# Performance work log

Measured on AMD Instinct MI355X. Metric: run time of the kernel, lower is better.

## Reference

```python
import jax, jax.numpy as jnp
import numpy as np

NUM_HEADS = 16
INACTIVE = 4          # cfg_comp.attention_heads_inactive
SIG_DIM = 64          # cfg_comp.attention_heads_signature_dim
MLP_HIDDEN = 512      # cfg_comp.attention_heads_inference_mlp_hidden


def setup_inputs() -> dict:
    key = jax.random.key(0)
    ks = jax.random.split(key, 16)
    S, B, E = 2048, 2, 1024
    def xavier(k, shape, gain=1.0):
        fan_in, fan_out = shape[1], shape[0]
        a = gain * np.sqrt(6.0 / (fan_in + fan_out))
        return jax.random.uniform(k, shape, jnp.float32, -a, a)
    g = 1.0 / np.sqrt(2.0)
    return {
        "query": jax.random.normal(ks[0], (S, B, E), jnp.float32),
        "q_w": xavier(ks[1], (E, E), g), "q_b": jnp.zeros((E,), jnp.float32),
        "k_w": xavier(ks[2], (E, E), g), "k_b": jnp.zeros((E,), jnp.float32),
        "v_w": xavier(ks[3], (E, E), g), "v_b": jnp.zeros((E,), jnp.float32),
        "out_w": xavier(ks[4], (E, E)), "out_b": jnp.zeros((E,), jnp.float32),
        "inf1_w": xavier(ks[5], (MLP_HIDDEN, E), np.sqrt(2.0)),
        "inf1_b": jnp.zeros((MLP_HIDDEN,), jnp.float32),
        "inf2_w": xavier(ks[6], (SIG_DIM, MLP_HIDDEN), np.sqrt(2.0)),
        "inf2_b": jnp.zeros((SIG_DIM,), jnp.float32),
        "head_sig": jax.random.normal(ks[7], (NUM_HEADS, SIG_DIM), jnp.float32)
                    * np.sqrt(2.0 / (NUM_HEADS + SIG_DIM)),
    }


def _head_mask(query, inf1_w, inf1_b, inf2_w, inf2_b, head_sig):
    # inference_masking_step: (S, B, E) -> binary mask (B, H, S)
    t = jax.nn.relu(query @ inf1_w.T + inf1_b)          # (S, B, hidden)
    t = t @ inf2_w.T + inf2_b                            # (S, B, sig)
    s = t @ head_sig.T                                   # (S, B, H) head scores
    keep = NUM_HEADS - INACTIVE
    kth = jax.lax.top_k(s, keep)[0][..., -1]             # (S, B) kth-largest score
    mask = (s >= kth[..., None]).astype(query.dtype)     # 1 at top-`keep` heads
    mask = jax.lax.stop_gradient(mask)                   # scatter of constants in torch
    return jnp.transpose(mask, (1, 2, 0))                # (B, H, S)


def reference(query, q_w, q_b, k_w, k_b, v_w, v_b, out_w, out_b,
              inf1_w, inf1_b, inf2_w, inf2_b, head_sig):
    S, B, E = query.shape
    H, D = NUM_HEADS, E // NUM_HEADS
    scaling = D ** (-0.5)

    q = (query @ q_w.T + q_b) * scaling                  # (S, B, E)
    k = query @ k_w.T + k_b
    v = query @ v_w.T + v_b
    # (S, B, E) -> (B, H, S, D)
    to_bhsd = lambda x: jnp.transpose(x.reshape(S, B, H, D), (1, 2, 0, 3))
    q, k, v = to_bhsd(q), to_bhsd(k), to_bhsd(v)

    attn = jax.nn.softmax(jnp.einsum("bhqd,bhkd->bhqk", q, k), axis=-1)
    o = jnp.einsum("bhqk,bhkd->bhqd", attn, v)           # (B, H, S, D)

    mask = _head_mask(query, inf1_w, inf1_b, inf2_w, inf2_b, head_sig)  # (B, H, S)
    o = o * mask[..., None]                              # gate per head per position

    out = jnp.transpose(o, (2, 0, 1, 3)).reshape(S, B, E)
    return out @ out_w.T + out_b
```

## Files before the change

kernel.cpp:

```cpp
#include <hip/hip_runtime.h>
#include <hip/hip_bf16.h>

#define S_LEN 2048
#define BATCH 2
#define EDIM 1024
#define NHEAD 16
#define DHEAD 64
#define HIDDEN 512
#define SIGD 64
#define KEEP 12

typedef __attribute__((ext_vector_type(8))) short bf16x8;
typedef __attribute__((ext_vector_type(4))) float f32x4;

static __device__ __forceinline__ float bf2f(short s) {
  unsigned int u = ((unsigned int)(unsigned short)s) << 16;
  float f; __builtin_memcpy(&f, &u, 4); return f;
}
static __device__ __forceinline__ short f2bf(float f) {
  unsigned int u; __builtin_memcpy(&u, &f, 4);
  u += 0x7fffu + ((u >> 16) & 1u);
  return (short)(u >> 16);
}

#if __has_builtin(__builtin_amdgcn_exp2f)
static __device__ __forceinline__ float fexp2(float x) { return __builtin_amdgcn_exp2f(x); }
#else
static __device__ __forceinline__ float fexp2(float x) { return exp2f(x); }
#endif

static __device__ __forceinline__ void gl_lds16(const short* g, short* l) {
  __builtin_amdgcn_global_load_lds(
      (const __attribute__((address_space(1))) unsigned int*)g,
      (__attribute__((address_space(3))) unsigned int*)l, 16, 0, 0);
}

template<int CTRL>
static __device__ __forceinline__ float dpp_movf(float x) {
  return __builtin_bit_cast(float, __builtin_amdgcn_update_dpp(
      0, __builtin_bit_cast(int, x), CTRL, 0xF, 0xF, true));
}
static __device__ __forceinline__ float row_max16(float v) {
  v = fmaxf(v, dpp_movf<0x128>(v));
  v = fmaxf(v, dpp_movf<0x124>(v));
  v = fmaxf(v, dpp_movf<0x122>(v));
  v = fmaxf(v, dpp_movf<0x121>(v));
  return v;
}
static __device__ __forceinline__ float row_sum16(float v) {
  v += dpp_movf<0x128>(v);
  v += dpp_movf<0x124>(v);
  v += dpp_movf<0x122>(v);
  v += dpp_movf<0x121>(v);
  return v;
}

__global__ __launch_bounds__(256) void cvt_all(
    const float* __restrict__ query, const float* __restrict__ inf1_w,
    const float* __restrict__ qw, const float* __restrict__ kw,
    const float* __restrict__ vw, const float* __restrict__ ow,
    short* __restrict__ qh, short* __restrict__ ql,
    short* __restrict__ w1h, short* __restrict__ w1l,
    short* __restrict__ Wq, short* __restrict__ Wk,
    short* __restrict__ Wv, short* __restrict__ Wo)
{
  int blk = blockIdx.x;
  if (blk < 4608) {
    const float* in; short *oh, *ol; int i;
    if (blk < 4096) { in = query;  oh = qh;  ol = ql;  i = (blk * 256 + threadIdx.x) * 4; }
    else            { in = inf1_w; oh = w1h; ol = w1l; i = ((blk - 4096) * 256 + threadIdx.x) * 4; }
    float4 f = *(const float4*)(in + i);
    union { short s[4]; uint2 v; } uh, ul;
    float x[4] = {f.x, f.y, f.z, f.w};
    #pragma unroll
    for (int u = 0; u < 4; ++u) {
      short h = f2bf(x[u]);
      uh.s[u] = h;
      ul.s[u] = f2bf(x[u] - bf2f(h));
    }
    *(uint2*)(oh + i) = uh.v;
    *(uint2*)(ol + i) = ul.v;
  } else {
    int t = blk - 4608;
    int mat = t >> 10, sub = t & 1023;
    const float* in = (mat == 0) ? qw : (mat == 1) ? kw : (mat == 2) ? vw : ow;
    short* out      = (mat == 0) ? Wq : (mat == 1) ? Wk : (mat == 2) ? Wv : Wo;
    int i = (sub * 256 + threadIdx.x) * 4;
    float4 f = *(const float4*)(in + i);
    union { short s[4]; uint2 v; } u;
    u.s[0] = f2bf(f.x); u.s[1] = f2bf(f.y); u.s[2] = f2bf(f.z); u.s[3] = f2bf(f.w);
    *(uint2*)(out + i) = u.v;
  }
}

template<bool F32OUT>
static __device__ __forceinline__ void gemm128_body(
    short* smem,
    const short* __restrict__ A, const short* __restrict__ B,
    const float* __restrict__ bias, void* __restrict__ outv,
    int row0, int col0, float scale)
{
  short* As = smem;
  short* Bs = smem + 128*32;
  const int tid  = threadIdx.x;
  const int wave = tid >> 6, lane = tid & 63;
  const int quad = lane >> 4, l16 = lane & 15;
  const int wr = wave >> 1, wc = wave & 1;
  const int lr = lane >> 2, lc8 = (lane & 3) * 8;

  const short* gA = A + (size_t)(row0 + wave*16 + lr) * EDIM + lc8;
  const short* gB = B + (size_t)(col0 + wave*16 + lr) * EDIM + lc8;
  short* lA = As + wave*512;
  short* lB = Bs + wave*512;

  f32x4 acc[4][4] = {};
  gl_lds16(gA, lA);  gl_lds16(gA + 64*EDIM, lA + 64*32);
  gl_lds16(gB, lB);  gl_lds16(gB + 64*EDIM, lB + 64*32);

  for (int k0 = 0; k0 < EDIM; k0 += 32) {
    __syncthreads();
    bf16x8 af[4], bfr[4];
    #pragma unroll
    for (int i = 0; i < 4; ++i)
      af[i] = *(const bf16x8*)&As[(wr*64 + i*16 + l16)*32 + quad*8];
    #pragma unroll
    for (int j = 0; j < 4; ++j)
      bfr[j] = *(const bf16x8*)&Bs[(wc*64 + j*16 + l16)*32 + quad*8];
    __syncthreads();
    if (k0 + 32 < EDIM) {
      const short* gA2 = gA + k0 + 32;
      const short* gB2 = gB + k0 + 32;
      gl_lds16(gA2, lA);  gl_lds16(gA2 + 64*EDIM, lA + 64*32);
      gl_lds16(gB2, lB);  gl_lds16(gB2 + 64*EDIM, lB + 64*32);
    }
    #pragma unroll
    for (int i = 0; i < 4; ++i)
      #pragma unroll
      for (int j = 0; j < 4; ++j)
        acc[i][j] = __builtin_amdgcn_mfma_f32_16x16x32_bf16(af[i], bfr[j], acc[i][j], 0, 0, 0);
  }
  #pragma unroll
  for (int j = 0; j < 4; ++j) {
    int col = col0 + wc*64 + j*16 + l16;
    float bv = bias[col];
    #pragma unroll
    for (int i = 0; i < 4; ++i) {
      int rowb = row0 + wr*64 + i*16 + quad*4;
      #pragma unroll
      for (int r = 0; r < 4; ++r) {
        float v = (acc[i][j][r] + bv) * scale;
        if constexpr (F32OUT) {
          ((float*)outv)[(size_t)(rowb + r) * EDIM + col] = v;
        } else {
          ((short*)outv)[(size_t)(rowb + r) * EDIM + col] = f2bf(v);
        }
      }
    }
  }
}

static __device__ __forceinline__ void gemm_t1_body(
    short* smem,
    const short* __restrict__ Agh, const short* __restrict__ Agl,
    const short* __restrict__ Bgh, const short* __restrict__ Bgl,
    const float* __restrict__ bias, float* __restrict__ T1,
    int row0, int col0)
{
  short* Ah = smem;
  short* Al = smem + 4096;
  short* Bh = smem + 8192;
  short* Bl = smem + 10240;
  const int tid  = threadIdx.x;
  const int wave = tid >> 6, lane = tid & 63;
  const int quad = lane >> 4, l16 = lane & 15;
  const int wr = wave >> 1, wc = wave & 1;
  const int lr = lane >> 2, lc8 = (lane & 3) * 8;

  const short* gAh = Agh + (size_t)(row0 + wave*16 + lr) * EDIM + lc8;
  const short* gAl = Agl + (size_t)(row0 + wave*16 + lr) * EDIM + lc8;
  const short* gBh = Bgh + (size_t)(col0 + wave*16 + lr) * EDIM + lc8;
  const short* gBl = Bgl + (size_t)(col0 + wave*16 + lr) * EDIM + lc8;
  short* lAh = Ah + wave*512;  short* lAl = Al + wave*512;
  short* lBh = Bh + wave*512;  short* lBl = Bl + wave*512;

  f32x4 acc[4][2] = {};
  gl_lds16(gAh, lAh);  gl_lds16(gAh + 64*EDIM, lAh + 64*32);
  gl_lds16(gAl, lAl);  gl_lds16(gAl + 64*EDIM, lAl + 64*32);
  gl_lds16(gBh, lBh);  gl_lds16(gBl, lBl);

  for (int k0 = 0; k0 < EDIM; k0 += 32) {
    __syncthreads();
    bf16x8 ah[4], al[4], bh[2], bl[2];
    #pragma unroll
    for (int i = 0; i < 4; ++i) {
      ah[i] = *(const bf16x8*)&Ah[(wr*64 + i*16 + l16)*32 + quad*8];
      al[i] = *(const bf16x8*)&Al[(wr*64 + i*16 + l16)*32 + quad*8];
    }
    #pragma unroll
    for (int j = 0; j < 2; ++j) {
      bh[j] = *(const bf16x8*)&Bh[(wc*32 + j*16 + l16)*32 + quad*8];
      bl[j] = *(const bf16x8*)&Bl[(wc*32 + j*16 + l16)*32 + quad*8];
    }
    __syncthreads();
    if (k0 + 32 < EDIM) {
      const short* p;
      p = gAh + k0 + 32;  gl_lds16(p, lAh);  gl_lds16(p + 64*EDIM, lAh + 64*32);
      p = gAl + k0 + 32;  gl_lds16(p, lAl);  gl_lds16(p + 64*EDIM, lAl + 64*32);
      gl_lds16(gBh + k0 + 32, lBh);  gl_lds16(gBl + k0 + 32, lBl);
    }
    #pragma unroll
    for (int i = 0; i < 4; ++i)
      #pragma unroll
      for (int j = 0; j < 2; ++j) {
        acc[i][j] = __builtin_amdgcn_mfma_f32_16x16x32_bf16(ah[i], bh[j], acc[i][j], 0, 0, 0);
        acc[i][j] = __builtin_amdgcn_mfma_f32_16x16x32_bf16(ah[i], bl[j], acc[i][j], 0, 0, 0);
        acc[i][j] = __builtin_amdgcn_mfma_f32_16x16x32_bf16(al[i], bh[j], acc[i][j], 0, 0, 0);
      }
  }
  #pragma unroll
  for (int j = 0; j < 2; ++j) {
    int col = col0 + wc*32 + j*16 + l16;
    float bv = bias[col];
    #pragma unroll
    for (int i = 0; i < 4; ++i) {
      int rowb = row0 + wr*64 + i*16 + quad*4;
      #pragma unroll
      for (int r = 0; r < 4; ++r)
        T1[(size_t)(rowb + r) * HIDDEN + col] = fmaxf(acc[i][j][r] + bv, 0.0f);
    }
  }
}

__global__ __launch_bounds__(256) void mega_gemm1(
    const short* __restrict__ qh, const short* __restrict__ ql,
    const short* __restrict__ w1h, const short* __restrict__ w1l,
    const float* __restrict__ inf1_b, float* __restrict__ T1,
    const short* __restrict__ Wq, const short* __restrict__ Wk,
    const short* __restrict__ Wv,
    const float* __restrict__ qb, const float* __restrict__ kb,
    const float* __restrict__ vb,
    short* __restrict__ Qp, short* __restrict__ Kp, short* __restrict__ Vp)
{
  __shared__ __attribute__((aligned(16))) short smem[12288];
  int blk = blockIdx.x;
  if ((blk & 3) == 3) {
    int id = blk >> 2;
    gemm_t1_body(smem, qh, ql, w1h, w1l, inf1_b, T1,
                 (id & 31) * 128, (id >> 5) * 64);
  } else {
    int id = (blk >> 2) * 3 + (blk & 3);
    int row0 = (id & 31) * 128;
    int rest = id >> 5;
    int mat = rest >> 3, cb = rest & 7;
    const short* B   = (mat == 0) ? Wq : (mat == 1) ? Wk : Wv;
    const float* bia = (mat == 0) ? qb : (mat == 1) ? kb : vb;
    short* out       = (mat == 0) ? Qp : (mat == 1) ? Kp : Vp;
    float scale      = (mat == 0) ? 0.18033688011112042f : 1.0f;
    gemm128_body<false>(smem, qh, B, bia, (void*)out, row0, cb * 128, scale);
  }
}

__global__ __launch_bounds__(256) void mid_kernel(
    const float* __restrict__ T1, const float* __restrict__ inf2_w,
    const float* __restrict__ inf2_b, const float* __restrict__ head_sig,
    float* __restrict__ maskbuf,
    const short* __restrict__ Vp, short* __restrict__ VT)
{
  __shared__ __attribute__((aligned(16))) float fsm[16*HIDDEN + 16*SIGD + 16*NHEAD];
  int blk = blockIdx.x;
  const int tid = threadIdx.x;
  if (blk < 256) {
    float (*t1s)[HIDDEN] = (float(*)[HIDDEN])fsm;
    float (*t2s)[SIGD]   = (float(*)[SIGD])(fsm + 16*HIDDEN);
    float (*ss)[NHEAD]   = (float(*)[NHEAD])(fsm + 16*HIDDEN + 16*SIGD);
    const int tok0 = blk * 16;
    {
      int row = tid >> 4, c0 = (tid & 15) * 32;
      const float* src = T1 + (size_t)(tok0 + row) * HIDDEN + c0;
      #pragma unroll
      for (int u = 0; u < 8; ++u)
        *(float4*)&t1s[row][c0 + u*4] = *(const float4*)(src + u*4);
    }
    __syncthreads();
    #pragma unroll
    for (int it = 0; it < 4; ++it) {
      int idx = tid + it * 256;
      int tok = idx >> 6, j = idx & 63;
      const float4* w4 = (const float4*)(inf2_w + (size_t)j * HIDDEN);
      const float4* t4 = (const float4*)(&t1s[tok][0]);
      float a = inf2_b[j];
      for (int k = 0; k < HIDDEN/4; ++k) {
        float4 wv = w4[k], tv = t4[k];
        a += tv.x*wv.x + tv.y*wv.y + tv.z*wv.z + tv.w*wv.w;
      }
      t2s[tok][j] = a;
    }
    __syncthreads();
    {
      int tok = tid >> 4, h = tid & 15;
      float a = 0.f;
      for (int d = 0; d < SIGD; ++d) a += t2s[tok][d] * head_sig[h*SIGD + d];
      ss[tok][h] = a;
    }
    __syncthreads();
    {
      int tok = tid >> 4, h = tid & 15;
      float sv = ss[tok][h];
      int cnt = 0;
      #pragma unroll
      for (int j = 0; j < NHEAD; ++j) cnt += (ss[tok][j] > sv) ? 1 : 0;
      int gt = tok0 + tok;
      int s = gt >> 1, b = gt & 1;
      maskbuf[((size_t)(b*NHEAD + h)) * S_LEN + s] = (cnt < KEEP) ? 1.0f : 0.0f;
    }
  } else {
    short (*tile)[72] = (short(*)[72])fsm;
    int t = blk - 256;
    const int s0 = (t & 31) * 64, e0 = ((t >> 5) & 15) * 64, b = t >> 9;
    {
      int sr = tid >> 2, ec = (tid & 3) * 16;
      const short* src = Vp + (size_t)(s0 + sr) * 2048 + b * 1024 + e0 + ec;
      *(uint4*)&tile[sr][ec]     = *(const uint4*)src;
      *(uint4*)&tile[sr][ec + 8] = *(const uint4*)(src + 8);
    }
    __syncthreads();
    {
      int er = tid >> 2, sc = (tid & 3) * 16;
      unsigned pack[8];
      #pragma unroll
      for (int u = 0; u < 8; ++u) {
        unsigned lo = (unsigned short)tile[sc + 2*u][er];
        unsigned hi = (unsigned short)tile[sc + 2*u + 1][er];
        pack[u] = lo | (hi << 16);
      }
      short* dst = VT + (size_t)(b * 1024 + e0 + er) * 2048 + s0 + sc;
      *(uint4*)(dst)     = *(uint4*)&pack[0];
      *(uint4*)(dst + 8) = *(uint4*)&pack[4];
    }
  }
}

__global__ __launch_bounds__(256) void flash_attn(
    short* QpOg, const short* __restrict__ Kp, const short* __restrict__ VT,
    const float* __restrict__ maskbuf)
{
  __shared__ __attribute__((aligned(16))) short smem[32768];
  short* KsL = smem;
  short* VtL = smem + 8192;
  short* PsB = smem + 16384;
  short* Qs  = smem + 16384;

  const int bh = blockIdx.x;
  const int b = bh >> 4, h = bh & 15;
  const int q0 = blockIdx.y * 128;
  const int tid = threadIdx.x;
  const int wave = tid >> 6, lane = tid & 63;
  const int quad = lane >> 4, l16 = lane & 15;
  const size_t colbase = (size_t)b * EDIM + h * DHEAD;
  const size_t rstride = (size_t)BATCH * EDIM;
  short* Psw = PsB + wave * 4096;

  {
    int row = tid >> 1;
    int cb  = (tid & 1) * 4;
    const short* src = QpOg + (size_t)(q0 + row) * rstride + colbase + cb * 8;
    #pragma unroll
    for (int u = 0; u < 4; ++u) {
      uint4 v = *(const uint4*)(src + u * 8);
      *(uint4*)&Qs[row * 64 + (((cb + u) ^ (row & 7)) * 8)] = v;
    }
  }
  __syncthreads();
  bf16x8 aq[2][2];
  #pragma unroll
  for (int h2 = 0; h2 < 2; ++h2)
    #pragma unroll
    for (int dh = 0; dh < 2; ++dh) {
      int row = wave * 32 + h2 * 16 + l16;
      aq[h2][dh] = *(const bf16x8*)&Qs[row * 64 + (((dh * 4 + quad) ^ (l16 & 7)) * 8)];
    }

  const int kxor = (lane & 7) ^ (lane >> 3);
  const short* gKbase = Kp + colbase + (size_t)(wave * 32 + (lane >> 3)) * rstride + kxor * 8;
  short* ldsK = KsL + wave * 2048;
  const int vrow_l = lane >> 4;
  short* ldsV = VtL + wave * 2048;

  float m_i[2][4], l_i[2][4];
  f32x4 oacc[2][4];
  #pragma unroll
  for (int h2 = 0; h2 < 2; ++h2)
    #pragma unroll
    for (int r = 0; r < 4; ++r) { m_i[h2][r] = -1e30f; l_i[h2][r] = 0.f; }
  #pragma unroll
  for (int h2 = 0; h2 < 2; ++h2)
    #pragma unroll
    for (int dt = 0; dt < 4; ++dt) oacc[h2][dt] = f32x4{0.f, 0.f, 0.f, 0.f};

  for (int kv0 = 0; kv0 < S_LEN; kv0 += 128) {
    __syncthreads();
    #pragma unroll
    for (int i = 0; i < 4; ++i) {
      gl_lds16(gKbase + (size_t)(kv0 + i * 8) * rstride, ldsK + i * 512);
      int vrow = wave * 16 + i * 4 + vrow_l;
      int vx = (lane & 15) ^ ((i & 1) * 4 + vrow_l);
      gl_lds16(VT + (size_t)(bh * 64 + vrow) * S_LEN + kv0 + vx * 8, ldsV + i * 512);
    }
    asm volatile("s_waitcnt vmcnt(0)" ::: "memory");
    __syncthreads();

    f32x4 sacc[2][8];
    #pragma unroll
    for (int h2 = 0; h2 < 2; ++h2)
      #pragma unroll
      for (int c = 0; c < 8; ++c) sacc[h2][c] = f32x4{0.f, 0.f, 0.f, 0.f};
    #pragma unroll
    for (int c = 0; c < 8; ++c) {
      const short* kr = &KsL[(c * 16 + l16) * 64];
      bf16x8 b0 = *(const bf16x8*)&kr[((quad     ^ (l16 & 7)) * 8)];
      bf16x8 b1 = *(const bf16x8*)&kr[(((4 + quad) ^ (l16 & 7)) * 8)];
      #pragma unroll
      for (int h2 = 0; h2 < 2; ++h2) {
        sacc[h2][c] = __builtin_amdgcn_mfma_f32_16x16x32_bf16(aq[h2][0], b0, sacc[h2][c], 0, 0, 0);
        sacc[h2][c] = __builtin_amdgcn_mfma_f32_16x16x32_bf16(aq[h2][1], b1, sacc[h2][c], 0, 0, 0);
      }
    }

    #pragma unroll
    for (int h2 = 0; h2 < 2; ++h2) {
      #pragma unroll
      for (int r = 0; r < 4; ++r) {
        float vmax = fmaxf(fmaxf(fmaxf(sacc[h2][0][r], sacc[h2][1][r]),
                                 fmaxf(sacc[h2][2][r], sacc[h2][3][r])),
                           fmaxf(fmaxf(sacc[h2][4][r], sacc[h2][5][r]),
                                 fmaxf(sacc[h2][6][r], sacc[h2][7][r])));
        vmax = row_max16(vmax);
        float mnew = fmaxf(m_i[h2][r], vmax);
        float alpha = fexp2(m_i[h2][r] - mnew);
        float rsum = 0.f;
        int row = h2 * 16 + quad * 4 + r;
        int sw = quad * 2 + (r >> 1);
        #pragma unroll
        for (int p = 0; p < 4; ++p) {
          float ea = fexp2(sacc[h2][2*p][r]   - mnew);
          float eb = fexp2(sacc[h2][2*p+1][r] - mnew);
          unsigned pk = __builtin_amdgcn_perm(
              __builtin_bit_cast(unsigned, eb),
              __builtin_bit_cast(unsigned, ea), 0x07060302u);
          short* pb = Psw + (p >> 1) * 2048 + row * 64;
          int c1 = ((2*p) & 3) * 2 + (l16 >> 3);
          int c2 = ((2*p+1) & 3) * 2 + (l16 >> 3);
          pb[((c1 ^ sw) * 8) + (l16 & 7)] = (short)(pk & 0xffffu);
          pb[((c2 ^ sw) * 8) + (l16 & 7)] = (short)(pk >> 16);
          rsum += ea + eb;
        }
        rsum = row_sum16(rsum);
        l_i[h2][r] = l_i[h2][r] * alpha + rsum;
        m_i[h2][r] = mnew;
        #pragma unroll
        for (int dt = 0; dt < 4; ++dt) oacc[h2][dt][r] *= alpha;
      }
    }
    asm volatile("s_waitcnt lgkmcnt(0)" ::: "memory");

    #pragma unroll
    for (int ks = 0; ks < 4; ++ks) {
      const short* p0 = Psw + (ks >> 1) * 2048;
      int pc = (((ks & 1) * 4 + quad) ^ (l16 >> 1)) * 8;
      bf16x8 ap0 = *(const bf16x8*)&p0[l16 * 64 + pc];
      bf16x8 ap1 = *(const bf16x8*)&p0[(16 + l16) * 64 + pc];
      #pragma unroll
      for (int dt = 0; dt < 4; ++dt) {
        bf16x8 bb = *(const bf16x8*)&VtL[(dt * 16 + l16) * 128 +
                                         (((ks * 4 + quad) ^ (l16 & 7)) * 8)];
        oacc[0][dt] = __builtin_amdgcn_mfma_f32_16x16x32_bf16(ap0, bb, oacc[0][dt], 0, 0, 0);
        oacc[1][dt] = __builtin_amdgcn_mfma_f32_16x16x32_bf16(ap1, bb, oacc[1][dt], 0, 0, 0);
      }
    }
  }

  #pragma unroll
  for (int h2 = 0; h2 < 2; ++h2) {
    #pragma unroll
    for (int r = 0; r < 4; ++r) {
      int s = q0 + wave * 32 + h2 * 16 + quad * 4 + r;
      float mk = maskbuf[((size_t)(b * NHEAD + h)) * S_LEN + s];
      float scale = mk / l_i[h2][r];
      short* dst = QpOg + (size_t)s * rstride + colbase;
      #pragma unroll
      for (int dt = 0; dt < 4; ++dt)
        dst[dt * 16 + l16] = f2bf(oacc[h2][dt][r] * scale);
    }
  }
}

__global__ __launch_bounds__(256) void gemm_out(
    const short* __restrict__ A, const short* __restrict__ W,
    const float* __restrict__ bias, float* __restrict__ out)
{
  __shared__ __attribute__((aligned(16))) short smem[8192];
  gemm128_body<true>(smem, A, W, bias, (void*)out,
                     blockIdx.x * 128, blockIdx.y * 128, 1.0f);
}

extern "C" void kernel_launch(void* const* d_in, const int* in_sizes, int n_in,
                              void* d_out, int out_size, void* d_ws, size_t ws_size,
                              hipStream_t stream)
{
  const float* query   = (const float*)d_in[0];
  const float* q_w     = (const float*)d_in[1];
  const float* q_b     = (const float*)d_in[2];
  const float* k_w     = (const float*)d_in[3];
  const float* k_b     = (const float*)d_in[4];
  const float* v_w     = (const float*)d_in[5];
  const float* v_b     = (const float*)d_in[6];
  const float* out_w   = (const float*)d_in[7];
  const float* out_b   = (const float*)d_in[8];
  const float* inf1_w  = (const float*)d_in[9];
  const float* inf1_b  = (const float*)d_in[10];
  const float* inf2_w  = (const float*)d_in[11];
  const float* inf2_b  = (const float*)d_in[12];
  const float* head_sig= (const float*)d_in[13];

  char* ws = (char*)d_ws;
  short* qh      = (short*)(ws);
  short* VTb     = (short*)(ws);
  short* ql      = (short*)(ws + (size_t)( 8u<<20));
  float* maskbuf = (float*)(ws + (size_t)( 8u<<20));
  short* Qp      = (short*)(ws + (size_t)(16u<<20));
  short* Kp      = (short*)(ws + (size_t)(24u<<20));
  short* Vp      = (short*)(ws + (size_t)(32u<<20));
  short* Wo      = (short*)(ws + (size_t)(40u<<20));
  char* ob = (char*)d_out;
  float* T1  = (float*)(ob);
  short* w1h = (short*)(ob + (size_t)( 8u<<20));
  short* w1l = (short*)(ob + (size_t)( 9u<<20));
  short* Wq  = (short*)(ob + (size_t)(10u<<20));
  short* Wk  = (short*)(ob + (size_t)(12u<<20));
  short* Wv  = (short*)(ob + (size_t)(14u<<20));
  float* out = (float*)d_out;

  dim3 blk(256);
  cvt_all<<<dim3(8704), blk, 0, stream>>>(query, inf1_w, q_w, k_w, v_w, out_w,
                                          qh, ql, w1h, w1l, Wq, Wk, Wv, Wo);
  mega_gemm1<<<dim3(1024), blk, 0, stream>>>(qh, ql, w1h, w1l, inf1_b, T1,
                                             Wq, Wk, Wv, q_b, k_b, v_b, Qp, Kp, Vp);
  mid_kernel<<<dim3(1280), blk, 0, stream>>>(T1, inf2_w, inf2_b, head_sig, maskbuf,
                                             Vp, VTb);
  flash_attn<<<dim3(32, 16), blk, 0, stream>>>(Qp, Kp, VTb, maskbuf);
  gemm_out<<<dim3(32, 8), blk, 0, stream>>>(Qp, Wo, out_b, out);
}
```

Measured before the change: 320.8 us.

## Transpose attention MFMA operands so each lane owns one query row

Swaps the A/B operands of the QK^T and PV MFMAs so the accumulator is laid out with query rows along lanes and keys along the register dimension. The online-softmax state then collapses to one max/sum per lane, row reductions need only two cross-lane bpermutes instead of a four-step DPP chain per row, and P is written to LDS with 8-byte vector stores instead of scalar 2-byte stores. The output epilogue also writes packed bf16 pairs. This adds ds_bpermute LDS traffic and changes the P swizzle layout, which must stay consistent with the PV reads.

```diff
diff --git a/kernel.cpp b/kernel.cpp
--- a/kernel.cpp
+++ b/kernel.cpp
@@ -35,24 +35,9 @@
       (__attribute__((address_space(3))) unsigned int*)l, 16, 0, 0);
 }
 
-template<int CTRL>
-static __device__ __forceinline__ float dpp_movf(float x) {
-  return __builtin_bit_cast(float, __builtin_amdgcn_update_dpp(
-      0, __builtin_bit_cast(int, x), CTRL, 0xF, 0xF, true));
-}
-static __device__ __forceinline__ float row_max16(float v) {
-  v = fmaxf(v, dpp_movf<0x128>(v));
-  v = fmaxf(v, dpp_movf<0x124>(v));
-  v = fmaxf(v, dpp_movf<0x122>(v));
-  v = fmaxf(v, dpp_movf<0x121>(v));
-  return v;
-}
-static __device__ __forceinline__ float row_sum16(float v) {
-  v += dpp_movf<0x128>(v);
-  v += dpp_movf<0x124>(v);
-  v += dpp_movf<0x122>(v);
-  v += dpp_movf<0x121>(v);
-  return v;
+static __device__ __forceinline__ float bperm_f(int idx, float v) {
+  return __builtin_bit_cast(float,
+      __builtin_amdgcn_ds_bpermute(idx, __builtin_bit_cast(int, v)));
 }
 
 __global__ __launch_bounds__(256) void cvt_all(
@@ -360,6 +345,9 @@
   const size_t rstride = (size_t)BATCH * EDIM;
   short* Psw = PsB + wave * 4096;
 
+  const int ix16 = (lane ^ 16) << 2;
+  const int ix32 = (lane ^ 32) << 2;
+
   {
     int row = tid >> 1;
     int cb  = (tid & 1) * 4;
@@ -386,12 +374,9 @@
   const int vrow_l = lane >> 4;
   short* ldsV = VtL + wave * 2048;
 
-  float m_i[2][4], l_i[2][4];
+  float m_i[2] = {-1e30f, -1e30f};
+  float l_i[2] = {0.f, 0.f};
   f32x4 oacc[2][4];
-  #pragma unroll
-  for (int h2 = 0; h2 < 2; ++h2)
-    #pragma unroll
-    for (int r = 0; r < 4; ++r) { m_i[h2][r] = -1e30f; l_i[h2][r] = 0.f; }
   #pragma unroll
   for (int h2 = 0; h2 < 2; ++h2)
     #pragma unroll
@@ -417,79 +402,87 @@
     #pragma unroll
     for (int c = 0; c < 8; ++c) {
       const short* kr = &KsL[(c * 16 + l16) * 64];
-      bf16x8 b0 = *(const bf16x8*)&kr[((quad     ^ (l16 & 7)) * 8)];
-      bf16x8 b1 = *(const bf16x8*)&kr[(((4 + quad) ^ (l16 & 7)) * 8)];
+      bf16x8 k0 = *(const bf16x8*)&kr[((quad     ^ (l16 & 7)) * 8)];
+      bf16x8 k1 = *(const bf16x8*)&kr[(((4 + quad) ^ (l16 & 7)) * 8)];
       #pragma unroll
       for (int h2 = 0; h2 < 2; ++h2) {
-        sacc[h2][c] = __builtin_amdgcn_mfma_f32_16x16x32_bf16(aq[h2][0], b0, sacc[h2][c], 0, 0, 0);
-        sacc[h2][c] = __builtin_amdgcn_mfma_f32_16x16x32_bf16(aq[h2][1], b1, sacc[h2][c], 0, 0, 0);
+        sacc[h2][c] = __builtin_amdgcn_mfma_f32_16x16x32_bf16(k0, aq[h2][0], sacc[h2][c], 0, 0, 0);
+        sacc[h2][c] = __builtin_amdgcn_mfma_f32_16x16x32_bf16(k1, aq[h2][1], sacc[h2][c], 0, 0, 0);
       }
     }
 
     #pragma unroll
     for (int h2 = 0; h2 < 2; ++h2) {
-      #pragma unroll
-      for (int r = 0; r < 4; ++r) {
-        float vmax = fmaxf(fmaxf(fmaxf(sacc[h2][0][r], sacc[h2][1][r]),
-                                 fmaxf(sacc[h2][2][r], sacc[h2][3][r])),
-                           fmaxf(fmaxf(sacc[h2][4][r], sacc[h2][5][r]),
-                                 fmaxf(sacc[h2][6][r], sacc[h2][7][r])));
-        vmax = row_max16(vmax);
-        float mnew = fmaxf(m_i[h2][r], vmax);
-        float alpha = fexp2(m_i[h2][r] - mnew);
-        float rsum = 0.f;
-        int row = h2 * 16 + quad * 4 + r;
-        int sw = quad * 2 + (r >> 1);
-        #pragma unroll
-        for (int p = 0; p < 4; ++p) {
-          float ea = fexp2(sacc[h2][2*p][r]   - mnew);
-          float eb = fexp2(sacc[h2][2*p+1][r] - mnew);
-          unsigned pk = __builtin_amdgcn_perm(
-              __builtin_bit_cast(unsigned, eb),
-              __builtin_bit_cast(unsigned, ea), 0x07060302u);
-          short* pb = Psw + (p >> 1) * 2048 + row * 64;
-          int c1 = ((2*p) & 3) * 2 + (l16 >> 3);
-          int c2 = ((2*p+1) & 3) * 2 + (l16 >> 3);
-          pb[((c1 ^ sw) * 8) + (l16 & 7)] = (short)(pk & 0xffffu);
-          pb[((c2 ^ sw) * 8) + (l16 & 7)] = (short)(pk >> 16);
-          rsum += ea + eb;
-        }
-        rsum = row_sum16(rsum);
-        l_i[h2][r] = l_i[h2][r] * alpha + rsum;
-        m_i[h2][r] = mnew;
-        #pragma unroll
-        for (int dt = 0; dt < 4; ++dt) oacc[h2][dt][r] *= alpha;
+      float vm = fmaxf(fmaxf(sacc[h2][0][0], sacc[h2][0][1]),
+                       fmaxf(sacc[h2][0][2], sacc[h2][0][3]));
+      #pragma unroll
+      for (int c = 1; c < 8; ++c)
+        vm = fmaxf(vm, fmaxf(fmaxf(sacc[h2][c][0], sacc[h2][c][1]),
+                             fmaxf(sacc[h2][c][2], sacc[h2][c][3])));
+      vm = fmaxf(vm, bperm_f(ix16, vm));
+      vm = fmaxf(vm, bperm_f(ix32, vm));
+      float mnew = fmaxf(m_i[h2], vm);
+      float alpha = fexp2(m_i[h2] - mnew);
+      float rs = 0.f;
+      short* pw = Psw + h2 * 2048 + l16 * 128 + (quad & 1) * 4;
+      #pragma unroll
+      for (int c = 0; c < 8; ++c) {
+        float e0 = fexp2(sacc[h2][c][0] - mnew);
+        float e1 = fexp2(sacc[h2][c][1] - mnew);
+        float e2 = fexp2(sacc[h2][c][2] - mnew);
+        float e3 = fexp2(sacc[h2][c][3] - mnew);
+        unsigned lo = __builtin_amdgcn_perm(
+            __builtin_bit_cast(unsigned, e1),
+            __builtin_bit_cast(unsigned, e0), 0x07060302u);
+        unsigned hi = __builtin_amdgcn_perm(
+            __builtin_bit_cast(unsigned, e3),
+            __builtin_bit_cast(unsigned, e2), 0x07060302u);
+        int ch = (c * 2 + (quad >> 1)) ^ (l16 & 7);
+        uint2 w2; w2.x = lo; w2.y = hi;
+        *(uint2*)(pw + ch * 8) = w2;
+        rs += (e0 + e1) + (e2 + e3);
+      }
+      rs += bperm_f(ix16, rs);
+      rs += bperm_f(ix32, rs);
+      l_i[h2] = l_i[h2] * alpha + rs;
+      m_i[h2] = mnew;
+      #pragma unroll
+      for (int dt = 0; dt < 4; ++dt) {
+        oacc[h2][dt][0] *= alpha; oacc[h2][dt][1] *= alpha;
+        oacc[h2][dt][2] *= alpha; oacc[h2][dt][3] *= alpha;
       }
     }
     asm volatile("s_waitcnt lgkmcnt(0)" ::: "memory");
 
     #pragma unroll
     for (int ks = 0; ks < 4; ++ks) {
-      const short* p0 = Psw + (ks >> 1) * 2048;
-      int pc = (((ks & 1) * 4 + quad) ^ (l16 >> 1)) * 8;
-      bf16x8 ap0 = *(const bf16x8*)&p0[l16 * 64 + pc];
-      bf16x8 ap1 = *(const bf16x8*)&p0[(16 + l16) * 64 + pc];
+      const short* pr = Psw + l16 * 128 + (((ks * 4 + quad) ^ (l16 & 7)) * 8);
+      bf16x8 ps0 = *(const bf16x8*)pr;
+      bf16x8 ps1 = *(const bf16x8*)(pr + 2048);
       #pragma unroll
       for (int dt = 0; dt < 4; ++dt) {
         bf16x8 bb = *(const bf16x8*)&VtL[(dt * 16 + l16) * 128 +
                                          (((ks * 4 + quad) ^ (l16 & 7)) * 8)];
-        oacc[0][dt] = __builtin_amdgcn_mfma_f32_16x16x32_bf16(ap0, bb, oacc[0][dt], 0, 0, 0);
-        oacc[1][dt] = __builtin_amdgcn_mfma_f32_16x16x32_bf16(ap1, bb, oacc[1][dt], 0, 0, 0);
+        oacc[0][dt] = __builtin_amdgcn_mfma_f32_16x16x32_bf16(bb, ps0, oacc[0][dt], 0, 0, 0);
+        oacc[1][dt] = __builtin_amdgcn_mfma_f32_16x16x32_bf16(bb, ps1, oacc[1][dt], 0, 0, 0);
       }
     }
   }
 
   #pragma unroll
   for (int h2 = 0; h2 < 2; ++h2) {
-    #pragma unroll
-    for (int r = 0; r < 4; ++r) {
-      int s = q0 + wave * 32 + h2 * 16 + quad * 4 + r;
-      float mk = maskbuf[((size_t)(b * NHEAD + h)) * S_LEN + s];
-      float scale = mk / l_i[h2][r];
-      short* dst = QpOg + (size_t)s * rstride + colbase;
-      #pragma unroll
-      for (int dt = 0; dt < 4; ++dt)
-        dst[dt * 16 + l16] = f2bf(oacc[h2][dt][r] * scale);
+    int q = q0 + wave * 32 + h2 * 16 + l16;
+    float mk = maskbuf[((size_t)(b * NHEAD + h)) * S_LEN + q];
+    float sc = mk / l_i[h2];
+    short* dst = QpOg + (size_t)q * rstride + colbase;
+    #pragma unroll
+    for (int dt = 0; dt < 4; ++dt) {
+      #pragma unroll
+      for (int p = 0; p < 2; ++p) {
+        unsigned lo = (unsigned short)f2bf(oacc[h2][dt][2*p]     * sc);
+        unsigned hi = (unsigned short)f2bf(oacc[h2][dt][2*p + 1] * sc);
+        *(unsigned*)(dst + dt*16 + quad*4 + 2*p) = lo | (hi << 16);
+      }
     }
   }
 }
```

Measured after the change: 309.8 us. -3.4%, faster.
